# Kernel tuning notes

Hardware: AMD Instinct MI355X
Metric: run time of the kernel (lower is better)

The kernel has to match this reference:

```python
import jax, jax.numpy as jnp
import numpy as np

N_NODES = 100000
N_EDGES = 1600000
DIM = 64


def setup_inputs() -> dict:
    key = jax.random.key(0)
    k1, k2, k3, k4 = jax.random.split(key, 4)
    x = jax.random.normal(k1, (N_NODES, DIM), dtype=jnp.float32)
    edge_index = jax.random.randint(k2, (2, N_EDGES), 0, N_NODES, dtype=jnp.int64)
    # GCNConv learned params (glorot-ish init)
    W = jax.random.normal(k3, (DIM, DIM), dtype=jnp.float32) / np.sqrt(DIM)
    b = jax.random.normal(k4, (DIM,), dtype=jnp.float32) * 0.01
    return {"x": x, "edge_index": edge_index, "W": W, "b": b}


def reference(x, edge_index, W, b):
    # GCNConv: x' = D^{-1/2} (A + I) D^{-1/2} (x W) + b  (add_self_loops=True)
    N = x.shape[0]
    h = x @ W  # [N, D]
    src, dst = edge_index[0], edge_index[1]
    ones = jnp.ones(src.shape, dtype=h.dtype)
    # degree including self loop
    deg = jax.ops.segment_sum(ones, dst, num_segments=N) + 1.0  # [N]
    dinv = jax.lax.rsqrt(deg)
    norm = dinv[src] * dinv[dst]  # [E] edge normalization
    # degree-normalized scatter-add aggregation over edges
    agg = jax.ops.segment_sum(h[src] * norm[:, None], dst, num_segments=N)
    # self-loop contribution: norm = 1/deg
    agg = agg + h * (dinv * dinv)[:, None]
    out = agg + b
    # epilogue: ReLU + dropout(p=0, eval) + residual
    out = jax.nn.relu(out)
    return x + out
```

## Files before the change

kernel.cpp:

```cpp
#include <hip/hip_runtime.h>

#define DIM 64
#define NPB 256
#define MAXBUCK 512
#define CHUNK 4096
#define BCAP 8192
#define BSTRIDE 16

__device__ __forceinline__ unsigned short f2bf(float v) {
    unsigned u = __float_as_uint(v);
    unsigned r = (u + 0x7fffu + ((u >> 16) & 1u)) >> 16;
    return (unsigned short)r;
}

__global__ void gcn_matmul(const float* __restrict__ x, const float* __restrict__ W,
                           unsigned short* __restrict__ hbf, int N) {
    __shared__ float Wl[DIM * DIM];
    __shared__ float xsT[DIM][68];
    int tid = threadIdx.x;
    for (int i = tid; i < 1024; i += 256)
        ((float4*)Wl)[i] = ((const float4*)W)[i];
    int node0 = blockIdx.x * 64;
#pragma unroll
    for (int rep = 0; rep < 4; ++rep) {
        int i = rep * 256 + tid;
        int nn = i >> 4;
        int c4 = (i & 15) * 4;
        int gn = node0 + nn;
        float4 v;
        if (gn < N) v = *(const float4*)(x + (long)gn * DIM + c4);
        else { v.x = v.y = v.z = v.w = 0.f; }
        xsT[c4 + 0][nn] = v.x;
        xsT[c4 + 1][nn] = v.y;
        xsT[c4 + 2][nn] = v.z;
        xsT[c4 + 3][nn] = v.w;
    }
    __syncthreads();

    int lane = tid & 63, wv_ = tid >> 6;
    int d4 = (lane & 15) * 4;
    int n0 = wv_ * 16 + (lane >> 4) * 4;
    float4 a0, a1, a2, a3;
    a0.x = a0.y = a0.z = a0.w = 0.f;
    a1.x = a1.y = a1.z = a1.w = 0.f;
    a2.x = a2.y = a2.z = a2.w = 0.f;
    a3.x = a3.y = a3.z = a3.w = 0.f;
#pragma unroll 2
    for (int k = 0; k < DIM; ++k) {
        float4 wr = *(const float4*)&Wl[k * DIM + d4];
        float4 xv = *(const float4*)&xsT[k][n0];
        a0.x += xv.x * wr.x; a0.y += xv.x * wr.y; a0.z += xv.x * wr.z; a0.w += xv.x * wr.w;
        a1.x += xv.y * wr.x; a1.y += xv.y * wr.y; a1.z += xv.y * wr.z; a1.w += xv.y * wr.w;
        a2.x += xv.z * wr.x; a2.y += xv.z * wr.y; a2.z += xv.z * wr.z; a2.w += xv.z * wr.w;
        a3.x += xv.w * wr.x; a3.y += xv.w * wr.y; a3.z += xv.w * wr.z; a3.w += xv.w * wr.w;
    }
#define STORE_NODE(j, aj)                                                   \
    {                                                                       \
        int gn = node0 + n0 + j;                                            \
        if (gn < N) {                                                       \
            uint2 p;                                                       \
            p.x = (unsigned)f2bf(aj.x) | ((unsigned)f2bf(aj.y) << 16);      \
            p.y = (unsigned)f2bf(aj.z) | ((unsigned)f2bf(aj.w) << 16);      \
            *(uint2*)(hbf + (long)gn * DIM + d4) = p;                       \
        }                                                                   \
    }
    STORE_NODE(0, a0) STORE_NODE(1, a1) STORE_NODE(2, a2) STORE_NODE(3, a3)
#undef STORE_NODE
}

__global__ void init_bcur(int* __restrict__ bcur, int nbuck) {
    int i = blockIdx.x * 256 + threadIdx.x;
    if (i < nbuck) bcur[i * BSTRIDE] = i * BCAP;
}

__global__ void bin_edges(const int* __restrict__ ei, int* __restrict__ bcur,
                          unsigned* __restrict__ binned, int E, int nbuck) {
    __shared__ int hist[MAXBUCK];
    int tid = threadIdx.x;
    long e0 = (long)blockIdx.x * CHUNK;
    for (int i = tid; i < nbuck; i += 256) hist[i] = 0;
    __syncthreads();
    int s[16], t[16];
#pragma unroll
    for (int it = 0; it < 16; ++it) {
        long e = e0 + it * 256 + tid;
        if (e < E) {
            s[it] = ei[e];
            t[it] = ei[E + e];
            atomicAdd(&hist[t[it] >> 8], 1);
        } else {
            s[it] = -1;
        }
    }
    __syncthreads();
    for (int i = tid; i < nbuck; i += 256) {
        int c = hist[i];
        hist[i] = c ? atomicAdd(&bcur[i * BSTRIDE], c) : 0;
    }
    __syncthreads();
#pragma unroll
    for (int it = 0; it < 16; ++it) {
        if (s[it] >= 0) {
            int b = t[it] >> 8;
            int p = atomicAdd(&hist[b], 1);
            binned[p] = ((unsigned)s[it] << 8) | (unsigned)(t[it] & 255);
        }
    }
}

__global__ void bucket_sort(const int* __restrict__ bcur, const unsigned* __restrict__ binned,
                            int* __restrict__ off, int* __restrict__ ncnt,
                            int* __restrict__ adj, float* __restrict__ dinv, int N) {
    __shared__ int lcur[NPB];
    __shared__ int sh[NPB];
    int bid = blockIdx.x, tid = threadIdx.x;
    int node0 = bid << 8;
    int e0 = bid * BCAP;
    int e1 = bcur[bid * BSTRIDE];
    if (tid < NPB) lcur[tid] = 0;
    __syncthreads();
    for (int e = e0 + tid; e < e1; e += 512)
        atomicAdd(&lcur[binned[e] & 255], 1);
    __syncthreads();
    int v = 0;
    if (tid < NPB) { v = lcur[tid]; sh[tid] = v; }
    __syncthreads();
    for (int d = 1; d < NPB; d <<= 1) {
        int t = (tid < NPB && tid >= d) ? sh[tid - d] : 0;
        __syncthreads();
        if (tid < NPB) sh[tid] += t;
        __syncthreads();
    }
    if (tid < NPB) {
        int excl = sh[tid] - v;
        lcur[tid] = excl;
        int node = node0 + tid;
        if (node < N) {
            off[node] = e0 + excl;
            ncnt[node] = v;
            dinv[node] = rsqrtf((float)v + 1.0f);
        }
    }
    __syncthreads();
    for (int e = e0 + tid; e < e1; e += 512) {
        unsigned u = binned[e];
        int p = atomicAdd(&lcur[u & 255], 1);
        adj[e0 + p] = (int)(u >> 8);
    }
}

__global__ void gather_agg(const int* __restrict__ off, const int* __restrict__ ncnt,
                           const int* __restrict__ adj,
                           const unsigned* __restrict__ hb, const float* __restrict__ dinv,
                           const float2* __restrict__ x2, const float2* __restrict__ b2,
                           float2* __restrict__ o2, int N) {
    int wid = threadIdx.x >> 6;
    int lane = threadIdx.x & 63;
    int nodeA = blockIdx.x * 8 + wid * 2;
    int nodeB = nodeA + 1;
    if (nodeA >= N) return;
    bool hasB = (nodeB < N);
    int sub = lane >> 5;
    int f = lane & 31;
    int startA = off[nodeA];
    int mA = ncnt[nodeA];
    int startB = hasB ? off[nodeB] : 0;
    int mB = hasB ? ncnt[nodeB] : 0;
    float dnA = dinv[nodeA];
    float dnB = hasB ? dinv[nodeB] : 0.f;
    unsigned usA = hb[(long)nodeA * 32 + f];
    unsigned usB = hasB ? hb[(long)nodeB * 32 + f] : 0u;
    float2 accA; accA.x = 0.f; accA.y = 0.f;
    float2 accB; accB.x = 0.f; accB.y = 0.f;

    int mmax = mA > mB ? mA : mB;
    for (int c = 0; c < mmax; c += 64) {
        int takeA = mA - c; if (takeA > 64) takeA = 64;
        int takeB = mB - c; if (takeB > 64) takeB = 64;
        int sA = (lane < takeA) ? adj[startA + c + lane] : 0;
        float wA = (lane < takeA) ? dinv[sA] : 0.f;
        int sB = (lane < takeB) ? adj[startB + c + lane] : 0;
        float wB = (lane < takeB) ? dinv[sB] : 0.f;
        int tmax = takeA > takeB ? takeA : takeB;
        for (int i = 0; i < tmax; i += 16) {
            unsigned uA0 = 0, uA1 = 0, uA2 = 0, uA3 = 0, uA4 = 0, uA5 = 0, uA6 = 0, uA7 = 0;
            unsigned uB0 = 0, uB1 = 0, uB2 = 0, uB3 = 0, uB4 = 0, uB5 = 0, uB6 = 0, uB7 = 0;
            float qA0 = 0, qA1 = 0, qA2 = 0, qA3 = 0, qA4 = 0, qA5 = 0, qA6 = 0, qA7 = 0;
            float qB0 = 0, qB1 = 0, qB2 = 0, qB3 = 0, qB4 = 0, qB5 = 0, qB6 = 0, qB7 = 0;
            if (i < takeA) {
                int i0 = i + 0 + sub, i1 = i + 2 + sub, i2 = i + 4 + sub, i3 = i + 6 + sub;
                int i4 = i + 8 + sub, i5 = i + 10 + sub, i6 = i + 12 + sub, i7 = i + 14 + sub;
                int t0 = __shfl(sA, i0), t1 = __shfl(sA, i1), t2 = __shfl(sA, i2), t3 = __shfl(sA, i3);
                int t4 = __shfl(sA, i4), t5 = __shfl(sA, i5), t6 = __shfl(sA, i6), t7 = __shfl(sA, i7);
                qA0 = __shfl(wA, i0); qA1 = __shfl(wA, i1); qA2 = __shfl(wA, i2); qA3 = __shfl(wA, i3);
                qA4 = __shfl(wA, i4); qA5 = __shfl(wA, i5); qA6 = __shfl(wA, i6); qA7 = __shfl(wA, i7);
                uA0 = hb[(long)t0 * 32 + f]; uA1 = hb[(long)t1 * 32 + f];
                uA2 = hb[(long)t2 * 32 + f]; uA3 = hb[(long)t3 * 32 + f];
                uA4 = hb[(long)t4 * 32 + f]; uA5 = hb[(long)t5 * 32 + f];
                uA6 = hb[(long)t6 * 32 + f]; uA7 = hb[(long)t7 * 32 + f];
            }
            if (i < takeB) {
                int i0 = i + 0 + sub, i1 = i + 2 + sub, i2 = i + 4 + sub, i3 = i + 6 + sub;
                int i4 = i + 8 + sub, i5 = i + 10 + sub, i6 = i + 12 + sub, i7 = i + 14 + sub;
                int t0 = __shfl(sB, i0), t1 = __shfl(sB, i1), t2 = __shfl(sB, i2), t3 = __shfl(sB, i3);
                int t4 = __shfl(sB, i4), t5 = __shfl(sB, i5), t6 = __shfl(sB, i6), t7 = __shfl(sB, i7);
                qB0 = __shfl(wB, i0); qB1 = __shfl(wB, i1); qB2 = __shfl(wB, i2); qB3 = __shfl(wB, i3);
                qB4 = __shfl(wB, i4); qB5 = __shfl(wB, i5); qB6 = __shfl(wB, i6); qB7 = __shfl(wB, i7);
                uB0 = hb[(long)t0 * 32 + f]; uB1 = hb[(long)t1 * 32 + f];
                uB2 = hb[(long)t2 * 32 + f]; uB3 = hb[(long)t3 * 32 + f];
                uB4 = hb[(long)t4 * 32 + f]; uB5 = hb[(long)t5 * 32 + f];
                uB6 = hb[(long)t6 * 32 + f]; uB7 = hb[(long)t7 * 32 + f];
            }
#define ACC(acc, u, q)                                                  \
            acc.x += __uint_as_float(u << 16) * q;                      \
            acc.y += __uint_as_float(u & 0xffff0000u) * q;
            ACC(accA, uA0, qA0) ACC(accA, uA1, qA1) ACC(accA, uA2, qA2) ACC(accA, uA3, qA3)
            ACC(accA, uA4, qA4) ACC(accA, uA5, qA5) ACC(accA, uA6, qA6) ACC(accA, uA7, qA7)
            ACC(accB, uB0, qB0) ACC(accB, uB1, qB1) ACC(accB, uB2, qB2) ACC(accB, uB3, qB3)
            ACC(accB, uB4, qB4) ACC(accB, uB5, qB5) ACC(accB, uB6, qB6) ACC(accB, uB7, qB7)
#undef ACC
        }
    }
    accA.x += __shfl_xor(accA.x, 32);
    accA.y += __shfl_xor(accA.y, 32);
    accB.x += __shfl_xor(accB.x, 32);
    accB.y += __shfl_xor(accB.y, 32);
    accA.x += __uint_as_float(usA << 16) * dnA;
    accA.y += __uint_as_float(usA & 0xffff0000u) * dnA;
    accB.x += __uint_as_float(usB << 16) * dnB;
    accB.y += __uint_as_float(usB & 0xffff0000u) * dnB;

    int wn = (lane < 32) ? nodeA : nodeB;
    float2 wacc = (lane < 32) ? accA : accB;
    float dnw = (lane < 32) ? dnA : dnB;
    if (wn < N) {
        long gi = (long)wn * 32 + f;
        float2 bb = b2[f];
        float2 xx = x2[gi];
        float2 r;
        r.x = xx.x + fmaxf(wacc.x * dnw + bb.x, 0.f);
        r.y = xx.y + fmaxf(wacc.y * dnw + bb.y, 0.f);
        o2[gi] = r;
    }
}

extern "C" void kernel_launch(void* const* d_in, const int* in_sizes, int n_in,
                              void* d_out, int out_size, void* d_ws, size_t ws_size,
                              hipStream_t stream) {
    const float* x = (const float*)d_in[0];
    const int* ei  = (const int*)d_in[1];
    const float* W = (const float*)d_in[2];
    const float* b = (const float*)d_in[3];
    float* out = (float*)d_out;

    int N = in_sizes[0] / DIM;
    int E = in_sizes[1] / 2;
    int nbuck = (N + NPB - 1) / NPB;

    char* ws = (char*)d_ws;
    size_t o = 0;
    unsigned short* hbf = (unsigned short*)(ws + o); o += (size_t)N * DIM * sizeof(unsigned short);
    float* dinv  = (float*)(ws + o); o += (size_t)N * sizeof(float);
    int*   off   = (int*)(ws + o);   o += (size_t)N * sizeof(int);
    int*   ncnt  = (int*)(ws + o);   o += (size_t)N * sizeof(int);
    int*   bcur  = (int*)(ws + o);   o += (size_t)nbuck * BSTRIDE * sizeof(int);
    unsigned* binned = (unsigned*)(ws + o); o += (size_t)nbuck * BCAP * sizeof(unsigned);
    int*   adj   = (int*)(ws + o);   o += (size_t)nbuck * BCAP * sizeof(int);

    gcn_matmul<<<(N + 63) / 64, 256, 0, stream>>>(x, W, hbf, N);
    init_bcur<<<(nbuck + 255) / 256, 256, 0, stream>>>(bcur, nbuck);
    bin_edges<<<(E + CHUNK - 1) / CHUNK, 256, 0, stream>>>(ei, bcur, binned, E, nbuck);
    bucket_sort<<<nbuck, 512, 0, stream>>>(bcur, binned, off, ncnt, adj, dinv, N);
    gather_agg<<<(N + 7) / 8, 256, 0, stream>>>(off, ncnt, adj, (const unsigned*)hbf, dinv,
                                                (const float2*)x, (const float2*)b,
                                                (float2*)out, N);
}
```

Measured before the change: 107.9 us.

## Fuse matmul and edge binning into one launch with memset-initialized bucket cursors

The independent x@W matmul and the edge-binning pass now run as disjoint block ranges of a single kernel that shares one LDS buffer. The init_bcur kernel is replaced by a hipMemsetAsync, with bucket cursors stored as relative offsets and the bucket base added at use. This is meant to cut launch overhead and let the compute-bound matmul blocks overlap with the atomic-heavy binning blocks. In exchange, each block reserves the larger matmul LDS footprint even when it only bins, which may lower occupancy for the binning blocks.

```diff
diff --git a/kernel.cpp b/kernel.cpp
--- a/kernel.cpp
+++ b/kernel.cpp
@@ -13,19 +13,57 @@
     return (unsigned short)r;
 }
 
-__global__ void gcn_matmul(const float* __restrict__ x, const float* __restrict__ W,
-                           unsigned short* __restrict__ hbf, int N) {
-    __shared__ float Wl[DIM * DIM];
-    __shared__ float xsT[DIM][68];
+__global__ void __launch_bounds__(256)
+fused_mm_bin(const float* __restrict__ x, const float* __restrict__ W,
+             unsigned short* __restrict__ hbf, int N,
+             const int* __restrict__ ei, int* __restrict__ bcur,
+             unsigned* __restrict__ binned, int E, int nbuck, int binB) {
+    __shared__ __align__(16) char buf[(DIM * DIM + DIM * 68) * 4];
     int tid = threadIdx.x;
+
+    if (blockIdx.x < binB) {
+        int* hist = (int*)buf;
+        long e0 = (long)blockIdx.x * CHUNK;
+        for (int i = tid; i < nbuck; i += 256) hist[i] = 0;
+        __syncthreads();
+        int s[16], t[16];
+#pragma unroll
+        for (int it = 0; it < 16; ++it) {
+            long e = e0 + it * 256 + tid;
+            if (e < E) {
+                s[it] = ei[e];
+                t[it] = ei[E + e];
+                atomicAdd(&hist[t[it] >> 8], 1);
+            } else {
+                s[it] = -1;
+            }
+        }
+        __syncthreads();
+        for (int i = tid; i < nbuck; i += 256) {
+            int c = hist[i];
+            hist[i] = c ? (i * BCAP + atomicAdd(&bcur[i * BSTRIDE], c)) : 0;
+        }
+        __syncthreads();
+#pragma unroll
+        for (int it = 0; it < 16; ++it) {
+            if (s[it] >= 0) {
+                int b = t[it] >> 8;
+                int p = atomicAdd(&hist[b], 1);
+                binned[p] = ((unsigned)s[it] << 8) | (unsigned)(t[it] & 255);
+            }
+        }
+        return;
+    }
+
+    float* Wl = (float*)buf;
+    float (*xsT)[68] = (float(*)[68])(buf + DIM * DIM * 4);
     for (int i = tid; i < 1024; i += 256)
         ((float4*)Wl)[i] = ((const float4*)W)[i];
-    int node0 = blockIdx.x * 64;
+    int node0 = (blockIdx.x - binB) * 64;
 #pragma unroll
     for (int rep = 0; rep < 4; ++rep) {
         int i = rep * 256 + tid;
-        int nn = i >> 4;
-        int c4 = (i & 15) * 4;
+        int nn = i >> 4, c4 = (i & 15) * 4;
         int gn = node0 + nn;
         float4 v;
         if (gn < N) v = *(const float4*)(x + (long)gn * DIM + c4);
@@ -68,46 +106,6 @@
 #undef STORE_NODE
 }
 
-__global__ void init_bcur(int* __restrict__ bcur, int nbuck) {
-    int i = blockIdx.x * 256 + threadIdx.x;
-    if (i < nbuck) bcur[i * BSTRIDE] = i * BCAP;
-}
-
-__global__ void bin_edges(const int* __restrict__ ei, int* __restrict__ bcur,
-                          unsigned* __restrict__ binned, int E, int nbuck) {
-    __shared__ int hist[MAXBUCK];
-    int tid = threadIdx.x;
-    long e0 = (long)blockIdx.x * CHUNK;
-    for (int i = tid; i < nbuck; i += 256) hist[i] = 0;
-    __syncthreads();
-    int s[16], t[16];
-#pragma unroll
-    for (int it = 0; it < 16; ++it) {
-        long e = e0 + it * 256 + tid;
-        if (e < E) {
-            s[it] = ei[e];
-            t[it] = ei[E + e];
-            atomicAdd(&hist[t[it] >> 8], 1);
-        } else {
-            s[it] = -1;
-        }
-    }
-    __syncthreads();
-    for (int i = tid; i < nbuck; i += 256) {
-        int c = hist[i];
-        hist[i] = c ? atomicAdd(&bcur[i * BSTRIDE], c) : 0;
-    }
-    __syncthreads();
-#pragma unroll
-    for (int it = 0; it < 16; ++it) {
-        if (s[it] >= 0) {
-            int b = t[it] >> 8;
-            int p = atomicAdd(&hist[b], 1);
-            binned[p] = ((unsigned)s[it] << 8) | (unsigned)(t[it] & 255);
-        }
-    }
-}
-
 __global__ void bucket_sort(const int* __restrict__ bcur, const unsigned* __restrict__ binned,
                             int* __restrict__ off, int* __restrict__ ncnt,
                             int* __restrict__ adj, float* __restrict__ dinv, int N) {
@@ -116,7 +114,7 @@
     int bid = blockIdx.x, tid = threadIdx.x;
     int node0 = bid << 8;
     int e0 = bid * BCAP;
-    int e1 = bcur[bid * BSTRIDE];
+    int e1 = e0 + bcur[bid * BSTRIDE];
     if (tid < NPB) lcur[tid] = 0;
     __syncthreads();
     for (int e = e0 + tid; e < e1; e += 512)
@@ -267,9 +265,12 @@
     unsigned* binned = (unsigned*)(ws + o); o += (size_t)nbuck * BCAP * sizeof(unsigned);
     int*   adj   = (int*)(ws + o);   o += (size_t)nbuck * BCAP * sizeof(int);
 
-    gcn_matmul<<<(N + 63) / 64, 256, 0, stream>>>(x, W, hbf, N);
-    init_bcur<<<(nbuck + 255) / 256, 256, 0, stream>>>(bcur, nbuck);
-    bin_edges<<<(E + CHUNK - 1) / CHUNK, 256, 0, stream>>>(ei, bcur, binned, E, nbuck);
+    int binB = (E + CHUNK - 1) / CHUNK;
+    int mmB  = (N + 63) / 64;
+
+    hipMemsetAsync(bcur, 0, (size_t)nbuck * BSTRIDE * sizeof(int), stream);
+    fused_mm_bin<<<binB + mmB, 256, 0, stream>>>(x, W, hbf, N, ei, bcur,
+                                                 binned, E, nbuck, binB);
     bucket_sort<<<nbuck, 512, 0, stream>>>(bcur, binned, off, ncnt, adj, dinv, N);
     gather_agg<<<(N + 7) / 8, 256, 0, stream>>>(off, ncnt, adj, (const unsigned*)hbf, dinv,
                                                 (const float2*)x, (const float2*)b,
```

Result: faster. 102.4 us, median of 2 (-5.1%).
